# Kernel optimization log

Measured on AMD Instinct MI355X. Metric: run time of the kernel, lower is better.

## Reference

```python
import jax, jax.numpy as jnp
import numpy as np

DIM = 32
D = DIM - 1  # 31
MARGIN = 0.85


def _lorentz_rotation(x, r_idx, rot_w):
    # rot_w: (R, D*D) raw embedding weights; full table is orthogonalized every call
    ww = jax.nn.gelu(rot_w, approximate=False).reshape(-1, D, D)  # (R, D, D): D Householder vectors per relation
    norm2 = jnp.sum(ww * ww, axis=-1)[..., None, None]            # (R, D, 1, 1)
    H = jnp.eye(D, dtype=x.dtype) - 2.0 * (ww[..., :, None] * ww[..., None, :]) / norm2  # (R, D, D, D)
    Hs = jnp.swapaxes(H, 0, 1)                                    # (D, R, D, D): scan over the D reflections
    Iw0 = jnp.broadcast_to(jnp.eye(D, dtype=x.dtype), (rot_w.shape[0], D, D))

    def step(c, Hi):
        return jnp.matmul(c, Hi), None

    Q, _ = jax.lax.scan(step, Iw0, Hs)                            # (R, D, D) orthogonal matrices
    Qb = Q[r_idx]                                                 # (B, D, D)
    x_rot = jnp.einsum('bnd,bdc->bnc', x[..., 1:], Qb)
    return jnp.concatenate([x[..., :1], x_rot], axis=-1)


def _lorentz_boost(x, r_idx, boost_w):
    ro = jnp.tanh(boost_w[r_idx]) / DIM                           # (B, D)
    v2 = jnp.sum(ro * ro, axis=-1)[:, None, None]                 # (B, 1, 1)
    zeta = 1.0 / (jnp.sqrt(1.0 - v2) + 1e-8)
    t = x[..., :1]                                                # (B, N, 1)
    r = x[..., 1:]                                                # (B, N, D)
    rob = ro[:, None, :]                                          # (B, 1, D)
    dot = jnp.sum(r * rob, axis=-1, keepdims=True)                # (B, N, 1) = <r, r_o>
    x0 = zeta * t - zeta * dot
    xr = -zeta * t * rob + r + (zeta - 1.0) / (v2 + 1e-9) * rob * dot
    return jnp.concatenate([x0, xr], axis=-1)


def setup_inputs() -> dict:
    key = jax.random.key(0)
    ks = jax.random.split(key, 8)
    B, N, E, R = 1024, 256, 500000, 2000
    std = 1.0 / float(np.sqrt(DIM))
    return {
        'u': jax.random.randint(ks[0], (B,), 0, E),
        'r': jax.random.randint(ks[1], (B,), 0, R),
        'v': jax.random.randint(ks[2], (B, N), 0, E),
        'emb': jax.random.normal(ks[3], (E, DIM), jnp.float32) * std,
        'bias_head': jnp.zeros((E,), jnp.float32),
        'bias_tail': jnp.zeros((E,), jnp.float32),
        'head_rot_w': jax.random.normal(ks[4], (R, D * D), jnp.float32),
        'head_boost_w': jax.random.normal(ks[5], (R, D), jnp.float32),
        'tail_rot_w': jax.random.normal(ks[6], (R, D * D), jnp.float32),
        'tail_boost_w': jax.random.normal(ks[7], (R, D), jnp.float32),
    }


def reference(u, r, v, emb, bias_head, bias_tail, head_rot_w, head_boost_w, tail_rot_w, tail_boost_w):
    h = emb[u][:, None, :]                                        # (B, 1, DIM)
    t = emb[v]                                                    # (B, N, DIM)
    th = _lorentz_boost(_lorentz_rotation(h, r, head_rot_w), r, head_boost_w)
    tt = _lorentz_boost(_lorentz_rotation(t, r, tail_rot_w), r, tail_boost_w)
    d = tt - th                                                   # (B, N, DIM)
    # Lorentz inner <d,d> = -d0^2 + sum_i di^2
    mkv = jnp.sum(d * d, axis=-1) - 2.0 * d[..., 0] ** 2          # (B, N)
    return MARGIN - mkv + jnp.tanh(bias_head[u])[:, None] + jnp.tanh(bias_tail[v])
```

## Files before the change

kernel.cpp:

```cpp
#include <hip/hip_runtime.h>

#define MARGIN 0.85f

__device__ __forceinline__ float gelu_exact(float x) {
    return 0.5f * x * (1.0f + erff(x * 0.7071067811865475f));
}

__global__ __launch_bounds__(256) void fused_kernel(
    const int* __restrict__ u_idx, const int* __restrict__ r_idx,
    const int* __restrict__ v_idx,
    const float* __restrict__ emb,
    const float* __restrict__ bias_head, const float* __restrict__ bias_tail,
    const float* __restrict__ head_rot_w, const float* __restrict__ head_boost_w,
    const float* __restrict__ tail_rot_w, const float* __restrict__ tail_boost_w,
    float* __restrict__ out)
{
    __shared__ float wrow[62][33];
    __shared__ float inv2n[62];
    __shared__ float hsld[32];
    __shared__ __align__(16) float wl[36];

    const int tid = threadIdx.x;
    const int b = blockIdx.x;
    const int r  = __builtin_amdgcn_readfirstlane(r_idx[b]);
    const int ub = __builtin_amdgcn_readfirstlane(u_idx[b]);

    const int vi = v_idx[(size_t)b * 256 + tid];

    const float* hw = head_rot_w + (size_t)r * 961;
    const float* tw = tail_rot_w + (size_t)r * 961;
    for (int e = tid; e < 961; e += 256) {
        const int row = e / 31;
        const int col = e - row * 31;
        wrow[row][col]      = gelu_exact(hw[e]);
        wrow[31 + row][col] = gelu_exact(tw[e]);
    }
    if (tid < 62) wrow[tid][31] = 0.0f;
    if (tid < 32) hsld[tid] = emb[(size_t)ub * 32 + tid];
    __syncthreads();

    if (tid < 62) {
        float n = 0.0f;
        #pragma unroll
        for (int k = 0; k < 31; ++k) n = fmaf(wrow[tid][k], wrow[tid][k], n);
        inv2n[tid] = 2.0f / n;
    }
    __syncthreads();

    const float4* ep = reinterpret_cast<const float4*>(emb + (size_t)vi * 32);
    const float4 e0 = ep[0], e1 = ep[1], e2 = ep[2], e3 = ep[3],
                 e4 = ep[4], e5 = ep[5], e6 = ep[6], e7 = ep[7];
    const float btl = bias_tail[vi];

    if (tid < 64) {
        const int k = tid & 31;
        const bool act = (k < 31);

        float x = act ? hsld[1 + k] : 0.0f;
        const float h0 = hsld[0];
        #pragma unroll
        for (int i = 0; i < 31; ++i) {
            const float w = wrow[i][k];
            float p = x * w;
            p += __shfl_xor(p, 1);
            p += __shfl_xor(p, 2);
            p += __shfl_xor(p, 4);
            p += __shfl_xor(p, 8);
            p += __shfl_xor(p, 16);
            x = fmaf(-(p * inv2n[i]), w, x);
        }

        const float roh = act ? tanhf(head_boost_w[(size_t)r * 31 + k]) * 0.03125f : 0.0f;
        float pv = roh * roh;
        float pd = x * roh;
        #pragma unroll
        for (int m = 1; m < 32; m <<= 1) {
            pv += __shfl_xor(pv, m);
            pd += __shfl_xor(pd, m);
        }
        const float zh = 1.0f / (sqrtf(1.0f - pv) + 1e-8f);
        const float ch = (zh - 1.0f) / (pv + 1e-9f);
        const float th  = fmaf(roh, ch * pd - zh * h0, x);
        const float th0 = zh * (h0 - pd);

        const float rot = act ? tanhf(tail_boost_w[(size_t)r * 31 + k]) * 0.03125f : 0.0f;
        float qv = rot * rot;
        float qd = rot * th;
        float qb = th * th;
        #pragma unroll
        for (int m = 1; m < 32; m <<= 1) {
            qv += __shfl_xor(qv, m);
            qd += __shfl_xor(qd, m);
            qb += __shfl_xor(qb, m);
        }
        const float zt = 1.0f / (sqrtf(1.0f - qv) + 1e-8f);
        const float ct = (zt - 1.0f) / (qv + 1e-9f);
        float y = 2.0f * fmaf(fmaf(zt, th0, ct * qd), rot, th);
        const float y0 = 2.0f * zt * (-th0 - qd);

        #pragma unroll
        for (int i = 30; i >= 0; --i) {
            const float w = wrow[31 + i][k];
            float p = y * w;
            p += __shfl_xor(p, 1);
            p += __shfl_xor(p, 2);
            p += __shfl_xor(p, 4);
            p += __shfl_xor(p, 8);
            p += __shfl_xor(p, 16);
            y = fmaf(-(p * inv2n[31 + i]), w, y);
        }

        if (tid < 32) {
            if (act) wl[1 + k] = y;
            else     wl[0] = y0;
        }
        if (tid == 0) {
            const float beta = qb - th0 * th0;
            wl[32] = MARGIN - beta + tanhf(bias_head[ub]);
        }
    }
    __syncthreads();

    float dotw = 0.0f, qsum = 0.0f;
    const float t0 = e0.x;
#define ACC(EV, WI)                                                       \
    {                                                                     \
        const float4 wq = *reinterpret_cast<const float4*>(&wl[4 * WI]);  \
        dotw = fmaf(EV.x, wq.x, dotw); dotw = fmaf(EV.y, wq.y, dotw);     \
        dotw = fmaf(EV.z, wq.z, dotw); dotw = fmaf(EV.w, wq.w, dotw);     \
        qsum = fmaf(EV.x, EV.x, qsum); qsum = fmaf(EV.y, EV.y, qsum);     \
        qsum = fmaf(EV.z, EV.z, qsum); qsum = fmaf(EV.w, EV.w, qsum);     \
    }
    ACC(e0, 0) ACC(e1, 1) ACC(e2, 2) ACC(e3, 3)
    ACC(e4, 4) ACC(e5, 5) ACC(e6, 6) ACC(e7, 7)
#undef ACC

    out[(size_t)b * 256 + tid] = wl[32] + dotw - qsum + 2.0f * t0 * t0 + tanhf(btl);
}

extern "C" void kernel_launch(void* const* d_in, const int* in_sizes, int n_in,
                              void* d_out, int out_size, void* d_ws, size_t ws_size,
                              hipStream_t stream) {
    (void)n_in; (void)out_size; (void)d_ws; (void)ws_size;
    const int B = in_sizes[0];
    fused_kernel<<<B, 256, 0, stream>>>(
        (const int*)d_in[0], (const int*)d_in[1], (const int*)d_in[2],
        (const float*)d_in[3], (const float*)d_in[4], (const float*)d_in[5],
        (const float*)d_in[6], (const float*)d_in[7],
        (const float*)d_in[8], (const float*)d_in[9],
        (float*)d_out);
}
```

Baseline: 133.9 us.

## Block Householder reflections in groups of four and use DPP reductions

Applies the 31 sequential Householder reflections in blocks of four. Pairwise inner products of the reflection vectors are precomputed in shared memory, so the four projections of each block can be reduced independently and then corrected with a small triangular solve. This shortens the serial dependency chain of cross-lane reductions. Shuffle-based reductions are replaced by DPP row operations plus a ds_swizzle. The boost norms are moved before the loops, and the row arrays are padded to 64 with a zero-weight dummy reflection.

```diff
diff --git a/kernel.cpp b/kernel.cpp
--- a/kernel.cpp
+++ b/kernel.cpp
@@ -4,6 +4,20 @@
 
 __device__ __forceinline__ float gelu_exact(float x) {
     return 0.5f * x * (1.0f + erff(x * 0.7071067811865475f));
+}
+
+template<int CTRL>
+__device__ __forceinline__ float dpp_add(float x) {
+    return x + __int_as_float(__builtin_amdgcn_update_dpp(
+        0, __float_as_int(x), CTRL, 0xF, 0xF, false));
+}
+__device__ __forceinline__ float reduce32(float x) {
+    x = dpp_add<0x121>(x);
+    x = dpp_add<0x122>(x);
+    x = dpp_add<0x124>(x);
+    x = dpp_add<0x128>(x);
+    x += __int_as_float(__builtin_amdgcn_ds_swizzle(__float_as_int(x), 0x401F));
+    return x;
 }
 
 __global__ __launch_bounds__(256) void fused_kernel(
@@ -15,8 +29,9 @@
     const float* __restrict__ tail_rot_w, const float* __restrict__ tail_boost_w,
     float* __restrict__ out)
 {
-    __shared__ float wrow[62][33];
-    __shared__ float inv2n[62];
+    __shared__ float wrow[64][33];
+    __shared__ float inv2n[64];
+    __shared__ float cd[2][8][6];
     __shared__ float hsld[32];
     __shared__ __align__(16) float wl[36];
 
@@ -33,17 +48,34 @@
         const int row = e / 31;
         const int col = e - row * 31;
         wrow[row][col]      = gelu_exact(hw[e]);
-        wrow[31 + row][col] = gelu_exact(tw[e]);
+        wrow[32 + row][col] = gelu_exact(tw[e]);
     }
-    if (tid < 62) wrow[tid][31] = 0.0f;
+    if (tid < 64) wrow[tid][31] = 0.0f;
+    if (tid >= 64 && tid < 97)   wrow[31][tid - 64] = 0.0f;
+    if (tid >= 128 && tid < 161) wrow[63][tid - 128] = 0.0f;
     if (tid < 32) hsld[tid] = emb[(size_t)ub * 32 + tid];
     __syncthreads();
 
-    if (tid < 62) {
+    if (tid < 64) {
         float n = 0.0f;
         #pragma unroll
         for (int k = 0; k < 31; ++k) n = fmaf(wrow[tid][k], wrow[tid][k], n);
-        inv2n[tid] = 2.0f / n;
+        inv2n[tid] = ((tid & 31) == 31) ? 0.0f : 2.0f / n;
+    }
+    if (tid >= 64 && tid < 160) {
+        const int t = tid - 64;
+        const int side = t / 48;
+        const int rem = t % 48;
+        const int g2 = rem / 6;
+        const int pr = rem % 6;
+        const int jj = (pr < 3) ? 0 : ((pr < 5) ? 1 : 2);
+        const int kk = (pr < 3) ? (pr + 1) : ((pr < 5) ? (pr - 1) : 3);
+        const int ra = side * 32 + g2 * 4 + jj;
+        const int rb = side * 32 + g2 * 4 + kk;
+        float s = 0.0f;
+        #pragma unroll
+        for (int q = 0; q < 31; ++q) s = fmaf(wrow[ra][q], wrow[rb][q], s);
+        cd[side][g2][pr] = s;
     }
     __syncthreads();
 
@@ -56,58 +88,62 @@
         const int k = tid & 31;
         const bool act = (k < 31);
 
+        const float roh = act ? tanhf(head_boost_w[(size_t)r * 31 + k]) * 0.03125f : 0.0f;
+        const float rot = act ? tanhf(tail_boost_w[(size_t)r * 31 + k]) * 0.03125f : 0.0f;
+        const float pv = reduce32(roh * roh);
+        const float qv = reduce32(rot * rot);
+        const float zh = 1.0f / (sqrtf(1.0f - pv) + 1e-8f);
+        const float ch = (zh - 1.0f) / (pv + 1e-9f);
+        const float zt = 1.0f / (sqrtf(1.0f - qv) + 1e-8f);
+        const float ct = (zt - 1.0f) / (qv + 1e-9f);
+
         float x = act ? hsld[1 + k] : 0.0f;
         const float h0 = hsld[0];
         #pragma unroll
-        for (int i = 0; i < 31; ++i) {
-            const float w = wrow[i][k];
-            float p = x * w;
-            p += __shfl_xor(p, 1);
-            p += __shfl_xor(p, 2);
-            p += __shfl_xor(p, 4);
-            p += __shfl_xor(p, 8);
-            p += __shfl_xor(p, 16);
-            x = fmaf(-(p * inv2n[i]), w, x);
+        for (int g2 = 0; g2 < 8; ++g2) {
+            const int base = g2 * 4;
+            const float w0 = wrow[base + 0][k];
+            const float w1 = wrow[base + 1][k];
+            const float w2 = wrow[base + 2][k];
+            const float w3 = wrow[base + 3][k];
+            float p0 = reduce32(x * w0);
+            float p1 = reduce32(x * w1);
+            float p2 = reduce32(x * w2);
+            float p3 = reduce32(x * w3);
+            const float* cg = cd[0][g2];
+            const float a0 = inv2n[base + 0] * p0;
+            const float a1 = inv2n[base + 1] * fmaf(-a0, cg[0], p1);
+            const float a2 = inv2n[base + 2] * (p2 - fmaf(a0, cg[1], a1 * cg[3]));
+            const float a3 = inv2n[base + 3] * (p3 - fmaf(a0, cg[2], fmaf(a1, cg[4], a2 * cg[5])));
+            x = x - (fmaf(a0, w0, a1 * w1) + fmaf(a2, w2, a3 * w3));
         }
 
-        const float roh = act ? tanhf(head_boost_w[(size_t)r * 31 + k]) * 0.03125f : 0.0f;
-        float pv = roh * roh;
-        float pd = x * roh;
-        #pragma unroll
-        for (int m = 1; m < 32; m <<= 1) {
-            pv += __shfl_xor(pv, m);
-            pd += __shfl_xor(pd, m);
-        }
-        const float zh = 1.0f / (sqrtf(1.0f - pv) + 1e-8f);
-        const float ch = (zh - 1.0f) / (pv + 1e-9f);
+        const float pd = reduce32(x * roh);
         const float th  = fmaf(roh, ch * pd - zh * h0, x);
         const float th0 = zh * (h0 - pd);
 
-        const float rot = act ? tanhf(tail_boost_w[(size_t)r * 31 + k]) * 0.03125f : 0.0f;
-        float qv = rot * rot;
-        float qd = rot * th;
-        float qb = th * th;
-        #pragma unroll
-        for (int m = 1; m < 32; m <<= 1) {
-            qv += __shfl_xor(qv, m);
-            qd += __shfl_xor(qd, m);
-            qb += __shfl_xor(qb, m);
-        }
-        const float zt = 1.0f / (sqrtf(1.0f - qv) + 1e-8f);
-        const float ct = (zt - 1.0f) / (qv + 1e-9f);
+        const float qd = reduce32(rot * th);
+        const float qb = reduce32(th * th);
         float y = 2.0f * fmaf(fmaf(zt, th0, ct * qd), rot, th);
         const float y0 = 2.0f * zt * (-th0 - qd);
 
         #pragma unroll
-        for (int i = 30; i >= 0; --i) {
-            const float w = wrow[31 + i][k];
-            float p = y * w;
-            p += __shfl_xor(p, 1);
-            p += __shfl_xor(p, 2);
-            p += __shfl_xor(p, 4);
-            p += __shfl_xor(p, 8);
-            p += __shfl_xor(p, 16);
-            y = fmaf(-(p * inv2n[31 + i]), w, y);
+        for (int g2 = 7; g2 >= 0; --g2) {
+            const int base = 32 + g2 * 4;
+            const float w0 = wrow[base + 0][k];
+            const float w1 = wrow[base + 1][k];
+            const float w2 = wrow[base + 2][k];
+            const float w3 = wrow[base + 3][k];
+            float p0 = reduce32(y * w0);
+            float p1 = reduce32(y * w1);
+            float p2 = reduce32(y * w2);
+            float p3 = reduce32(y * w3);
+            const float* cg = cd[1][g2];
+            const float b3 = inv2n[base + 3] * p3;
+            const float b2 = inv2n[base + 2] * fmaf(-b3, cg[5], p2);
+            const float b1 = inv2n[base + 1] * (p1 - fmaf(b3, cg[4], b2 * cg[3]));
+            const float b0 = inv2n[base + 0] * (p0 - fmaf(b3, cg[2], fmaf(b2, cg[1], b1 * cg[0])));
+            y = y - (fmaf(b0, w0, b1 * w1) + fmaf(b2, w2, b3 * w3));
         }
 
         if (tid < 32) {
```

Result: faster. 128.2 us (-4.3%).
